# Performance work log

Measured on AMD Instinct MI355X. Metric: run time of the kernel, lower is better.

## Reference

```python
import jax, jax.numpy as jnp
import numpy as np

BATCH, SEQ, IN_DIM, HID = 4096, 512, 64, 10


def setup_inputs() -> dict:
    key = jax.random.key(0)
    k1, k2, k3, k4, k5 = jax.random.split(key, 5)
    return {
        "x": jax.random.normal(k1, (BATCH, SEQ, IN_DIM), dtype=jnp.float32),
        "W_ih": jax.random.normal(k2, (4 * HID, IN_DIM), dtype=jnp.float32) * 0.1,
        "W_hh": jax.random.normal(k3, (4 * HID, HID), dtype=jnp.float32) * 0.1,
        "b_ih": jax.random.normal(k4, (4 * HID,), dtype=jnp.float32) * 0.1,
        "b_hh": jax.random.normal(k5, (4 * HID,), dtype=jnp.float32) * 0.1,
    }


def _lstm_scan(x, W_ih, W_hh, b_ih, b_hh):
    B = x.shape[0]
    H = W_hh.shape[1]
    # Precompute input projections for all timesteps in one big GEMM: [T, B, 4H]
    xg = jnp.einsum('bti,gi->tbg', x, W_ih) + b_ih + b_hh

    def step(carry, xt_g):
        h, c = carry
        gates = xt_g + h @ W_hh.T  # [B, 4H]
        i, f, g, o = jnp.split(gates, 4, axis=-1)  # PyTorch gate order i,f,g,o
        i = jax.nn.sigmoid(i)
        f = jax.nn.sigmoid(f)
        g = jnp.tanh(g)
        o = jax.nn.sigmoid(o)
        c_new = f * c + i * g
        h_new = o * jnp.tanh(c_new)
        return (h_new, c_new), h_new

    h0 = jnp.zeros((B, H), dtype=x.dtype)
    c0 = jnp.zeros((B, H), dtype=x.dtype)
    (h_last, _), hs = jax.lax.scan(step, (h0, c0), xg)
    return hs.transpose(1, 0, 2), h_last  # [B, T, H], [B, H]


def reference(x, W_ih, W_hh, b_ih, b_hh):
    output, h_last = _lstm_scan(x, W_ih, W_hh, b_ih, b_hh)
    return (output, h_last)
```

## Files before the change

kernel.cpp:

```cpp
#include <hip/hip_runtime.h>
#include <hip/hip_fp16.h>

typedef float f32x2 __attribute__((ext_vector_type(2)));

#define TSEQ 512
#define IND 64
#define HID 10
#define NG 40
#define BATCH 4096
#define ROWS (BATCH * TSEQ)
#define RPB 256
#define LSTRIDE 21
#define CSTR 68

#define L2E   1.4426950408889634f
#define L2E2  2.8853900817779268f

__device__ __forceinline__ float lane_f(float v, int l) {
  return __builtin_bit_cast(float, __builtin_amdgcn_readlane(__builtin_bit_cast(int, v), l));
}

__global__ __launch_bounds__(256) void input_proj(
    const float* __restrict__ x, const float* __restrict__ W_ih,
    const float* __restrict__ b_ih, const float* __restrict__ b_hh,
    unsigned int* __restrict__ xg)
{
  __shared__ __align__(16) unsigned int st[RPB * LSTRIDE];
  float* const fin = (float*)st;
  const int tid = threadIdx.x;
  const int lr  = tid & 63;
  const int myc = tid >> 6;
  const long long rowbase = (long long)blockIdx.x * RPB;

  f32x2 xr[32];
#pragma unroll 1
  for (int c = 0; c < 4; ++c) {
    const float4* src = (const float4*)(x + (rowbase + (long long)c * 64) * IND);
#pragma unroll
    for (int p = 0; p < 4; ++p) {
      int j = tid + 256 * p;
      float4 v = src[j];
      int r = j >> 4, m = (j & 15) << 2;
      *(float4*)&fin[r * CSTR + m] = v;
    }
    __syncthreads();
    if (myc == c) {
#pragma unroll
      for (int i = 0; i < 16; ++i) {
        float4 v = *(const float4*)&fin[lr * CSTR + 4 * i];
        xr[2*i]   = f32x2{v.x, v.y};
        xr[2*i+1] = f32x2{v.z, v.w};
      }
    }
    __syncthreads();
  }

#pragma unroll 1
  for (int gc = 0; gc < 10; ++gc) {
    const f32x2* w0 = (const f32x2*)(W_ih + (4*gc + 0) * IND);
    const f32x2* w1 = (const f32x2*)(W_ih + (4*gc + 1) * IND);
    const f32x2* w2 = (const f32x2*)(W_ih + (4*gc + 2) * IND);
    const f32x2* w3 = (const f32x2*)(W_ih + (4*gc + 3) * IND);
    f32x2 a0 = {0.f, 0.f}, a1 = {0.f, 0.f}, a2 = {0.f, 0.f}, a3 = {0.f, 0.f};
#pragma unroll
    for (int k = 0; k < 32; ++k) {
      a0 = __builtin_elementwise_fma(xr[k], w0[k], a0);
      a1 = __builtin_elementwise_fma(xr[k], w1[k], a1);
      a2 = __builtin_elementwise_fma(xr[k], w2[k], a2);
      a3 = __builtin_elementwise_fma(xr[k], w3[k], a3);
    }
    float s0 = ((4*gc + 0) / 10 == 2) ? -L2E2 : -L2E;
    float s1 = ((4*gc + 1) / 10 == 2) ? -L2E2 : -L2E;
    float s2 = ((4*gc + 2) / 10 == 2) ? -L2E2 : -L2E;
    float s3 = ((4*gc + 3) / 10 == 2) ? -L2E2 : -L2E;
    float g0 = (a0.x + a0.y + b_ih[4*gc + 0] + b_hh[4*gc + 0]) * s0;
    float g1 = (a1.x + a1.y + b_ih[4*gc + 1] + b_hh[4*gc + 1]) * s1;
    float g2 = (a2.x + a2.y + b_ih[4*gc + 2] + b_hh[4*gc + 2]) * s2;
    float g3 = (a3.x + a3.y + b_ih[4*gc + 3] + b_hh[4*gc + 3]) * s3;
    _Float16 q0 = (_Float16)g0, q1 = (_Float16)g1, q2 = (_Float16)g2, q3 = (_Float16)g3;
    unsigned p01 = (unsigned)__builtin_bit_cast(unsigned short, q0) |
                   ((unsigned)__builtin_bit_cast(unsigned short, q1) << 16);
    unsigned p23 = (unsigned)__builtin_bit_cast(unsigned short, q2) |
                   ((unsigned)__builtin_bit_cast(unsigned short, q3) << 16);
    st[tid * LSTRIDE + 2*gc]     = p01;
    st[tid * LSTRIDE + 2*gc + 1] = p23;
  }
  __syncthreads();

  const long long obase = (long long)blockIdx.x * (RPB * 20);
#pragma unroll
  for (int it = 0; it < 5; ++it) {
    int d0 = it * 1024 + tid * 4;
    int r = d0 / 20, m = d0 % 20;
    const unsigned* p = &st[r * LSTRIDE + m];
    uint4 vv; vv.x = p[0]; vv.y = p[1]; vv.z = p[2]; vv.w = p[3];
    *(uint4*)(xg + obase + d0) = vv;
  }
}

__global__ __launch_bounds__(64) void lstm_rec(
    const _Float16* __restrict__ xg, const float* __restrict__ W_hh,
    float* __restrict__ out_seq, float* __restrict__ out_h)
{
  __shared__ float hbuf[80];
  const int b    = blockIdx.x;
  const int lane = threadIdx.x;
  const int g    = lane < NG ? lane : NG - 1;
  const int li   = lane < NG ? lane : 0;
  const int tt   = g / HID;

  const float aMul = (tt == 2) ? 2.0f : 1.0f;
  const float aAdd = (tt == 2) ? -1.0f : 0.0f;
  const float mscale = (tt == 2) ? -L2E2 : -L2E;

  float whh[HID];
#pragma unroll
  for (int u = 0; u < HID; ++u) whh[u] = W_hh[g * HID + u] * mscale;

  const _Float16* xr = xg + (size_t)b * TSEQ * NG + li;
  float* orow = out_seq + (size_t)b * TSEQ * HID;

  float h = 0.0f, c = 0.0f;
  _Float16 xb[8];
#pragma unroll
  for (int j = 0; j < 8; ++j) xb[j] = xr[j * NG];

  for (int t0 = 0; t0 < TSEQ; t0 += 8) {
#pragma unroll
    for (int j = 0; j < 8; ++j) {
      float acc = (float)xb[j];
      if (t0 + 8 < TSEQ) xb[j] = xr[(t0 + j + 8) * NG];

#pragma unroll
      for (int u = 0; u < HID; ++u)
        acc = fmaf(lane_f(h, u), whh[u], acc);

      float e   = __builtin_amdgcn_exp2f(acc);
      float s   = __builtin_amdgcn_rcpf(1.0f + e);
      float act = fmaf(aMul, s, aAdd);

      float iv = __shfl(act, lane);
      float fv = __shfl(act, lane + 10);
      float gv = __shfl(act, lane + 20);
      float ov = __shfl(act, lane + 30);

      c = fmaf(fv, c, iv * gv);
      float e2 = __builtin_amdgcn_exp2f(-L2E2 * c);
      float th = fmaf(2.0f, __builtin_amdgcn_rcpf(1.0f + e2), -1.0f);
      h = ov * th;

      if (lane < HID) hbuf[j * HID + lane] = h;
    }
    __syncthreads();
    if (lane < 40) {
      float2 p; p.x = hbuf[2 * lane]; p.y = hbuf[2 * lane + 1];
      ((float2*)(orow + t0 * HID))[lane] = p;
    }
    __syncthreads();
  }
  if (lane < HID) out_h[(size_t)b * HID + lane] = h;
}

extern "C" void kernel_launch(void* const* d_in, const int* in_sizes, int n_in,
                              void* d_out, int out_size, void* d_ws, size_t ws_size,
                              hipStream_t stream) {
  const float* x    = (const float*)d_in[0];
  const float* W_ih = (const float*)d_in[1];
  const float* W_hh = (const float*)d_in[2];
  const float* b_ih = (const float*)d_in[3];
  const float* b_hh = (const float*)d_in[4];

  unsigned int* xg = (unsigned int*)d_ws;
  float* out_seq = (float*)d_out;
  float* out_h   = (float*)d_out + (size_t)BATCH * TSEQ * HID;

  input_proj<<<dim3(ROWS / RPB), dim3(RPB), 0, stream>>>(x, W_ih, b_ih, b_hh, xg);
  lstm_rec<<<dim3(BATCH), dim3(64), 0, stream>>>((const _Float16*)xg, W_hh, out_seq, out_h);
}
```

Before: 1.049 ms.

## Pack four batch rows per wavefront with per-unit gate computation in recurrence

The recurrence kernel now handles four batch sequences per 64-lane wave, with 16 lanes per sequence. Each lane computes all four gates for one hidden unit, which removes the four cross-lane shuffles per step, and the hidden state is exchanged through LDS instead of readlane. The input projection reorders its gate output so each unit's i,f,g,o values sit together as a uint2, and it stages W_ih in LDS. The risks are four times the FMA and transcendental work per lane, reliance on wave-synchronous LDS visibility without barriers, and a quarter as many blocks in the recurrence launch.

```diff
diff --git a/kernel.cpp b/kernel.cpp
--- a/kernel.cpp
+++ b/kernel.cpp
@@ -16,8 +16,11 @@
 #define L2E   1.4426950408889634f
 #define L2E2  2.8853900817779268f
 
-__device__ __forceinline__ float lane_f(float v, int l) {
-  return __builtin_bit_cast(float, __builtin_amdgcn_readlane(__builtin_bit_cast(int, v), l));
+static __device__ __forceinline__ float h2f_lo(unsigned v) {
+  return (float)__builtin_bit_cast(_Float16, (unsigned short)(v & 0xffffu));
+}
+static __device__ __forceinline__ float h2f_hi(unsigned v) {
+  return (float)__builtin_bit_cast(_Float16, (unsigned short)(v >> 16));
 }
 
 __global__ __launch_bounds__(256) void input_proj(
@@ -26,11 +29,14 @@
     unsigned int* __restrict__ xg)
 {
   __shared__ __align__(16) unsigned int st[RPB * LSTRIDE];
+  __shared__ __align__(16) float wlds[NG * IND];
   float* const fin = (float*)st;
   const int tid = threadIdx.x;
   const int lr  = tid & 63;
   const int myc = tid >> 6;
   const long long rowbase = (long long)blockIdx.x * RPB;
+
+  for (int i = tid; i < NG * IND; i += 256) wlds[i] = W_ih[i];
 
   f32x2 xr[32];
 #pragma unroll 1
@@ -56,11 +62,11 @@
   }
 
 #pragma unroll 1
-  for (int gc = 0; gc < 10; ++gc) {
-    const f32x2* w0 = (const f32x2*)(W_ih + (4*gc + 0) * IND);
-    const f32x2* w1 = (const f32x2*)(W_ih + (4*gc + 1) * IND);
-    const f32x2* w2 = (const f32x2*)(W_ih + (4*gc + 2) * IND);
-    const f32x2* w3 = (const f32x2*)(W_ih + (4*gc + 3) * IND);
+  for (int u = 0; u < HID; ++u) {
+    const f32x2* w0 = (const f32x2*)&wlds[(u     ) * IND];
+    const f32x2* w1 = (const f32x2*)&wlds[(u + 10) * IND];
+    const f32x2* w2 = (const f32x2*)&wlds[(u + 20) * IND];
+    const f32x2* w3 = (const f32x2*)&wlds[(u + 30) * IND];
     f32x2 a0 = {0.f, 0.f}, a1 = {0.f, 0.f}, a2 = {0.f, 0.f}, a3 = {0.f, 0.f};
 #pragma unroll
     for (int k = 0; k < 32; ++k) {
@@ -69,21 +75,17 @@
       a2 = __builtin_elementwise_fma(xr[k], w2[k], a2);
       a3 = __builtin_elementwise_fma(xr[k], w3[k], a3);
     }
-    float s0 = ((4*gc + 0) / 10 == 2) ? -L2E2 : -L2E;
-    float s1 = ((4*gc + 1) / 10 == 2) ? -L2E2 : -L2E;
-    float s2 = ((4*gc + 2) / 10 == 2) ? -L2E2 : -L2E;
-    float s3 = ((4*gc + 3) / 10 == 2) ? -L2E2 : -L2E;
-    float g0 = (a0.x + a0.y + b_ih[4*gc + 0] + b_hh[4*gc + 0]) * s0;
-    float g1 = (a1.x + a1.y + b_ih[4*gc + 1] + b_hh[4*gc + 1]) * s1;
-    float g2 = (a2.x + a2.y + b_ih[4*gc + 2] + b_hh[4*gc + 2]) * s2;
-    float g3 = (a3.x + a3.y + b_ih[4*gc + 3] + b_hh[4*gc + 3]) * s3;
+    float g0 = (a0.x + a0.y + b_ih[u     ] + b_hh[u     ]) * (-L2E);
+    float g1 = (a1.x + a1.y + b_ih[u + 10] + b_hh[u + 10]) * (-L2E);
+    float g2 = (a2.x + a2.y + b_ih[u + 20] + b_hh[u + 20]) * (-L2E2);
+    float g3 = (a3.x + a3.y + b_ih[u + 30] + b_hh[u + 30]) * (-L2E);
     _Float16 q0 = (_Float16)g0, q1 = (_Float16)g1, q2 = (_Float16)g2, q3 = (_Float16)g3;
     unsigned p01 = (unsigned)__builtin_bit_cast(unsigned short, q0) |
                    ((unsigned)__builtin_bit_cast(unsigned short, q1) << 16);
     unsigned p23 = (unsigned)__builtin_bit_cast(unsigned short, q2) |
                    ((unsigned)__builtin_bit_cast(unsigned short, q3) << 16);
-    st[tid * LSTRIDE + 2*gc]     = p01;
-    st[tid * LSTRIDE + 2*gc + 1] = p23;
+    st[tid * LSTRIDE + 2*u]     = p01;
+    st[tid * LSTRIDE + 2*u + 1] = p23;
   }
   __syncthreads();
 
@@ -99,66 +101,75 @@
 }
 
 __global__ __launch_bounds__(64) void lstm_rec(
-    const _Float16* __restrict__ xg, const float* __restrict__ W_hh,
+    const uint2* __restrict__ xg, const float* __restrict__ W_hh,
     float* __restrict__ out_seq, float* __restrict__ out_h)
 {
-  __shared__ float hbuf[80];
-  const int b    = blockIdx.x;
+  __shared__ __align__(16) float hb[8][4][16];
   const int lane = threadIdx.x;
-  const int g    = lane < NG ? lane : NG - 1;
-  const int li   = lane < NG ? lane : 0;
-  const int tt   = g / HID;
+  const int bi = lane >> 4;
+  const int u  = lane & 15;
+  const int uc = (u < HID) ? u : HID - 1;
+  const size_t b = (size_t)blockIdx.x * 4 + bi;
 
-  const float aMul = (tt == 2) ? 2.0f : 1.0f;
-  const float aAdd = (tt == 2) ? -1.0f : 0.0f;
-  const float mscale = (tt == 2) ? -L2E2 : -L2E;
+  float wi[HID], wf[HID], wg[HID], wo[HID];
+#pragma unroll
+  for (int k = 0; k < HID; ++k) {
+    wi[k] = W_hh[(uc     ) * HID + k] * (-L2E);
+    wf[k] = W_hh[(uc + 10) * HID + k] * (-L2E);
+    wg[k] = W_hh[(uc + 20) * HID + k] * (-L2E2);
+    wo[k] = W_hh[(uc + 30) * HID + k] * (-L2E);
+  }
 
-  float whh[HID];
+  const uint2* xp = xg + b * TSEQ * HID + uc;
+  float h = 0.f, c = 0.f;
+  hb[7][bi][u] = 0.f;
+
+  uint2 xb[8];
 #pragma unroll
-  for (int u = 0; u < HID; ++u) whh[u] = W_hh[g * HID + u] * mscale;
-
-  const _Float16* xr = xg + (size_t)b * TSEQ * NG + li;
-  float* orow = out_seq + (size_t)b * TSEQ * HID;
-
-  float h = 0.0f, c = 0.0f;
-  _Float16 xb[8];
-#pragma unroll
-  for (int j = 0; j < 8; ++j) xb[j] = xr[j * NG];
+  for (int j = 0; j < 8; ++j) xb[j] = xp[(size_t)j * HID];
 
   for (int t0 = 0; t0 < TSEQ; t0 += 8) {
 #pragma unroll
     for (int j = 0; j < 8; ++j) {
-      float acc = (float)xb[j];
-      if (t0 + 8 < TSEQ) xb[j] = xr[(t0 + j + 8) * NG];
+      uint2 xv = xb[j];
+      if (t0 + 8 < TSEQ) xb[j] = xp[(size_t)(t0 + j + 8) * HID];
+      float ai = h2f_lo(xv.x);
+      float af = h2f_hi(xv.x);
+      float ag = h2f_lo(xv.y);
+      float ao = h2f_hi(xv.y);
 
+      const float* hr = &hb[(j + 7) & 7][bi][0];
+      float4 h03 = *(const float4*)hr;
+      float4 h47 = *(const float4*)(hr + 4);
+      float2 h89 = *(const float2*)(hr + 8);
+      float hhv[HID] = {h03.x, h03.y, h03.z, h03.w,
+                        h47.x, h47.y, h47.z, h47.w, h89.x, h89.y};
 #pragma unroll
-      for (int u = 0; u < HID; ++u)
-        acc = fmaf(lane_f(h, u), whh[u], acc);
+      for (int k = 0; k < HID; ++k) {
+        ai = fmaf(hhv[k], wi[k], ai);
+        af = fmaf(hhv[k], wf[k], af);
+        ag = fmaf(hhv[k], wg[k], ag);
+        ao = fmaf(hhv[k], wo[k], ao);
+      }
+      float i_ = __builtin_amdgcn_rcpf(1.f + __builtin_amdgcn_exp2f(ai));
+      float f_ = __builtin_amdgcn_rcpf(1.f + __builtin_amdgcn_exp2f(af));
+      float g_ = fmaf(2.f, __builtin_amdgcn_rcpf(1.f + __builtin_amdgcn_exp2f(ag)), -1.f);
+      float o_ = __builtin_amdgcn_rcpf(1.f + __builtin_amdgcn_exp2f(ao));
 
-      float e   = __builtin_amdgcn_exp2f(acc);
-      float s   = __builtin_amdgcn_rcpf(1.0f + e);
-      float act = fmaf(aMul, s, aAdd);
-
-      float iv = __shfl(act, lane);
-      float fv = __shfl(act, lane + 10);
-      float gv = __shfl(act, lane + 20);
-      float ov = __shfl(act, lane + 30);
-
-      c = fmaf(fv, c, iv * gv);
-      float e2 = __builtin_amdgcn_exp2f(-L2E2 * c);
-      float th = fmaf(2.0f, __builtin_amdgcn_rcpf(1.0f + e2), -1.0f);
-      h = ov * th;
-
-      if (lane < HID) hbuf[j * HID + lane] = h;
+      c = fmaf(f_, c, i_ * g_);
+      float th = fmaf(2.f, __builtin_amdgcn_rcpf(1.f + __builtin_amdgcn_exp2f(-L2E2 * c)), -1.f);
+      h = o_ * th;
+      hb[j][bi][u] = h;
     }
-    __syncthreads();
-    if (lane < 40) {
-      float2 p; p.x = hbuf[2 * lane]; p.y = hbuf[2 * lane + 1];
-      ((float2*)(orow + t0 * HID))[lane] = p;
+#pragma unroll
+    for (int k = 0; k < 5; ++k) {
+      int e = lane + 64 * k;
+      int bb = e / 80, rem = e - bb * 80;
+      int jj = rem / 10, uu = rem - jj * 10;
+      out_seq[((size_t)(blockIdx.x * 4 + bb) * TSEQ + t0) * HID + rem] = hb[jj][bb][uu];
     }
-    __syncthreads();
   }
-  if (lane < HID) out_h[(size_t)b * HID + lane] = h;
+  if (u < HID) out_h[b * HID + u] = h;
 }
 
 extern "C" void kernel_launch(void* const* d_in, const int* in_sizes, int n_in,
@@ -175,5 +186,5 @@
   float* out_h   = (float*)d_out + (size_t)BATCH * TSEQ * HID;
 
   input_proj<<<dim3(ROWS / RPB), dim3(RPB), 0, stream>>>(x, W_ih, b_ih, b_hh, xg);
-  lstm_rec<<<dim3(BATCH), dim3(64), 0, stream>>>((const _Float16*)xg, W_hh, out_seq, out_h);
+  lstm_rec<<<dim3(BATCH / 4), dim3(64), 0, stream>>>((const uint2*)xg, W_hh, out_seq, out_h);
 }
```

New measurement: 929.8 us. 1.13x faster.
